# Kernel tuning notes

Measured on AMD Instinct MI355X. Metric: run time of the kernel, lower is better.

The kernel has to match this reference:

```python
import jax, jax.numpy as jnp
import numpy as np

WEIGHT = 1.0  # init kwarg: loss weight
N = 4096
D_FEAT = 128


def _pairwise_dist(x):
    # x: [n, d] -> D: [n, n] Euclidean distances (safe sqrt for grad at 0)
    sq = jnp.sum(x * x, axis=-1)
    d2 = sq[:, None] + sq[None, :] - 2.0 * (x @ x.T)
    d2 = jnp.maximum(d2, 0.0)
    pos = d2 > 1e-12
    return jnp.where(pos, jnp.sqrt(jnp.where(pos, d2, 1.0)), 0.0)


def _prim_mst(D):
    # Vectorized Prim: returns (parents, children) of the n-1 MST edges.
    # filtration value (VR complex truncated at max_dimension=1).
    n = D.shape[0]
    INF = jnp.finfo(D.dtype).max
    visited0 = jnp.zeros(n, dtype=bool).at[0].set(True)
    mind0 = D[0]
    parent0 = jnp.zeros(n, dtype=jnp.int32)

    def step(carry, _):
        visited, mind, parent = carry
        j = jnp.argmin(jnp.where(visited, INF, mind))
        pj = parent[j]
        visited = visited.at[j].set(True)
        better = (D[j] < mind) & (~visited)
        mind = jnp.where(better, D[j], mind)
        parent = jnp.where(better, j, parent)
        return (visited, mind, parent), (pj, j.astype(jnp.int32))

    _, (pjs, js) = jax.lax.scan(step, (visited0, mind0, parent0), None, length=n - 1)
    return pjs, js


def _h1_persistence(x):
    # H1 diagram for VR complex with max_dimension=1: a 1-cycle is born when a
    # non-MST edge appears; with no 2-simplices it never dies, so deaths are
    # capped at the maximal filtration value. Persistence = cap - birth.
    n = x.shape[0]
    D = _pairwise_dist(x)
    pjs, js = _prim_mst(D)
    tree = jnp.zeros((n, n), dtype=bool)
    tree = tree.at[pjs, js].set(True)
    tree = tree | tree.T
    iu = np.triu_indices(n, 1)  # static indices
    births = D[iu]              # [n*(n-1)/2]
    is_tree = tree[iu]
    cap = jnp.max(D)
    # tree edges are H0 (not H1): give them zero persistence (diagonal points)
    return jnp.where(is_tree, 0.0, cap - births)


def _wasserstein_1d(p1, p2):
    # 1-Wasserstein between equal-size persistence multisets via sorted matching
    # (deaths share a common cap per diagram, so matching by sorted persistence).
    return jnp.sum(jnp.abs(jnp.sort(p1) - jnp.sort(p2)))


def setup_inputs() -> dict:
    key = jax.random.key(0)
    k1, k2, k3, k4 = jax.random.split(key, 4)
    return {
        "graph1_features": jax.random.normal(k1, (N, D_FEAT), dtype=jnp.float32),
        "graph1_edges": jax.random.randint(k2, (2, 8 * N), 0, N, dtype=jnp.int64),
        "graph2_features": jax.random.normal(k3, (N, D_FEAT), dtype=jnp.float32),
        "graph2_edges": jax.random.randint(k4, (2, 8 * N), 0, N, dtype=jnp.int64),
    }


def reference(graph1_features, graph1_edges, graph2_features, graph2_edges):
    # edge tensors are unused: the torch forward builds VR complexes from the
    # point clouds only (build_from_points), matching the original module.
    p1 = _h1_persistence(graph1_features)
    p2 = _h1_persistence(graph2_features)
    return WEIGHT * _wasserstein_1d(p1, p2)
```

## Files before the change

### kernel.cpp

```cpp
#include <hip/hip_runtime.h>
#include <stdint.h>

#define NN 4096
#define DF 128
#define NBINS 16384
#define NSLAB 256
#define BORUVKA_ROUNDS 12

typedef __attribute__((ext_vector_type(8))) short short8;
typedef __attribute__((ext_vector_type(4))) float floatx4;
typedef __attribute__((ext_vector_type(4))) unsigned short ushort4_t;
typedef __attribute__((ext_vector_type(4))) int int4_t;

__device__ __forceinline__ unsigned bin_of(float v, float scale) {
  if (v < 0.f) v = 0.f;
  unsigned b = (unsigned)(v * scale);
  return b >= (unsigned)NBINS ? (unsigned)(NBINS - 1) : b;
}

__device__ __forceinline__ void gload16(const unsigned short* g, unsigned short* l) {
  __builtin_amdgcn_global_load_lds(
      (const __attribute__((address_space(1))) void*)g,
      (__attribute__((address_space(3))) void*)l, 16, 0, 0);
}

__global__ void k_rownorm(const float* __restrict__ x1, const float* __restrict__ x2,
                          float* __restrict__ sq) {
  int i = blockIdx.x * blockDim.x + threadIdx.x;
  if (i >= 2 * NN) return;
  const float* x = (i < NN) ? x1 : x2;
  int r = i & (NN - 1);
  const float* row = x + (size_t)r * DF;
  float s = 0.f;
  for (int k = 0; k < DF; ++k) s += row[k] * row[k];
  sq[i] = s;
}

__global__ __launch_bounds__(256) void k_bound(const float* __restrict__ sq,
                                               float* __restrict__ hdrf) {
  int t = threadIdx.x;
  float m = 0.f;
  for (int i = t; i < 2 * NN; i += 256) m = fmaxf(m, sq[i]);
  for (int off = 32; off > 0; off >>= 1) m = fmaxf(m, __shfl_down(m, off, 64));
  __shared__ float wm[4];
  if ((t & 63) == 0) wm[t >> 6] = m;
  __syncthreads();
  if (t == 0) {
    float mm = fmaxf(fmaxf(wm[0], wm[1]), fmaxf(wm[2], wm[3]));
    float dbound = 2.f * sqrtf(mm);
    hdrf[2] = 65535.f / dbound;
    hdrf[3] = dbound / 65535.f;
  }
}

__global__ void k_split(const float* __restrict__ x1, const float* __restrict__ x2,
                        unsigned short* __restrict__ xh, unsigned short* __restrict__ xl) {
  int i = blockIdx.x * blockDim.x + threadIdx.x;
  if (i >= 2 * NN * DF) return;
  const float* x = (i < NN * DF) ? x1 : x2;
  float v = x[i & (NN * DF - 1)];
  unsigned u = __float_as_uint(v);
  unsigned hu = u & 0xffff0000u;
  float hf = __uint_as_float(hu);
  float lf = v - hf;
  unsigned lu = __float_as_uint(lf) & 0xffff0000u;
  xh[i] = (unsigned short)(hu >> 16);
  xl[i] = (unsigned short)(lu >> 16);
}

#define SJ 136
__global__ __launch_bounds__(256) void k_dist(const unsigned short* __restrict__ Xhi,
                                              const unsigned short* __restrict__ Xlo,
                                              const float* __restrict__ sq,
                                              const float* __restrict__ hdrf,
                                              unsigned short* __restrict__ Qbase,
                                              unsigned* __restrict__ caps) {
  int bi = blockIdx.y, bj = blockIdx.x;
  if (bi > bj) return;
  bool offdiag = (bi != bj);
  int g = blockIdx.z;
  const unsigned short* xh = Xhi + (size_t)g * NN * DF;
  const unsigned short* xl = Xlo + (size_t)g * NN * DF;
  const float* sqg = sq + g * NN;
  unsigned short* Q = Qbase + (size_t)g * NN * NN;
  float qs = hdrf[2];
  int t = threadIdx.x;
  int w = t >> 6, lane = t & 63;
  int m = lane & 15, quad = lane >> 4;
  int iw = (w >> 1) * 64, jw = (w & 1) * 64;
  int i0 = bi * 128 + iw;
  int j0 = bj * 128 + jw;

  __shared__ __align__(16) unsigned short SB[128 * SJ];

  int baseRow = (w < 2) ? bi * 128 : bj * 128;
  const unsigned short* src = (w == 0 || w == 2) ? xh : xl;
  unsigned short* ldsPiece = &SB[w * 4096];
  int rsub = lane >> 2;
  int kpart = (lane & 3) ^ ((lane >> 3) & 3);

  int fr = (quad ^ ((m >> 1) & 3)) << 3;

  floatx4 acc[4][4];
#pragma unroll
  for (int ti = 0; ti < 4; ++ti)
#pragma unroll
    for (int tj = 0; tj < 4; ++tj) acc[ti][tj] = (floatx4){0.f, 0.f, 0.f, 0.f};

  for (int s = 0; s < 4; ++s) {
    int kc = s * 32;
    if (s) __syncthreads();
#pragma unroll
    for (int i = 0; i < 8; ++i) {
      const unsigned short* gp =
          src + (size_t)(baseRow + i * 16 + rsub) * DF + kc + kpart * 8;
      gload16(gp, &ldsPiece[i * 512]);
    }
    __syncthreads();
    short8 ah[4], al[4], bh[4], bl[4];
#pragma unroll
    for (int ti = 0; ti < 4; ++ti) {
      int ra = (iw + ti * 16 + m) * 32 + fr;
      int rb = (jw + ti * 16 + m) * 32 + fr;
      ah[ti] = *(const short8*)&SB[ra];
      al[ti] = *(const short8*)&SB[4096 + ra];
      bh[ti] = *(const short8*)&SB[8192 + rb];
      bl[ti] = *(const short8*)&SB[12288 + rb];
    }
#pragma unroll
    for (int ti = 0; ti < 4; ++ti)
#pragma unroll
      for (int tj = 0; tj < 4; ++tj) {
        acc[ti][tj] = __builtin_amdgcn_mfma_f32_16x16x32_bf16(ah[ti], bh[tj], acc[ti][tj], 0, 0, 0);
        acc[ti][tj] = __builtin_amdgcn_mfma_f32_16x16x32_bf16(ah[ti], bl[tj], acc[ti][tj], 0, 0, 0);
        acc[ti][tj] = __builtin_amdgcn_mfma_f32_16x16x32_bf16(al[ti], bh[tj], acc[ti][tj], 0, 0, 0);
      }
  }

  float sqj[4];
#pragma unroll
  for (int tj = 0; tj < 4; ++tj) sqj[tj] = sqg[j0 + tj * 16 + m];
  float mx = 0.f;
  ushort4_t qv[4][4];
#pragma unroll
  for (int ti = 0; ti < 4; ++ti) {
    int ib = i0 + ti * 16 + quad * 4;
    float sqiv[4];
#pragma unroll
    for (int r = 0; r < 4; ++r) sqiv[r] = sqg[ib + r];
#pragma unroll
    for (int tj = 0; tj < 4; ++tj) {
#pragma unroll
      for (int r = 0; r < 4; ++r) {
        float d2 = sqiv[r] + sqj[tj] - 2.f * acc[ti][tj][r];
        d2 = fmaxf(d2, 0.f);
        float d = (d2 > 1e-12f) ? sqrtf(d2) : 0.f;
        mx = fmaxf(mx, d);
        unsigned q = (unsigned)(d * qs + 0.5f);
        if (q > 65535u) q = 65535u;
        qv[ti][tj][r] = (unsigned short)q;
      }
    }
  }

  __syncthreads();
  unsigned short* T = SB;
  int sub = t >> 4, l16 = t & 15;

#pragma unroll
  for (int ti = 0; ti < 4; ++ti) {
    int il = iw + ti * 16 + quad * 4;
#pragma unroll
    for (int tj = 0; tj < 4; ++tj) {
      int jl = jw + tj * 16 + m;
      *(ushort4_t*)&T[jl * SJ + il] = qv[ti][tj];
    }
  }
  __syncthreads();
#pragma unroll
  for (int k = 0; k < 8; ++k) {
    int jl = k * 16 + sub;
    int4_t v = *(const int4_t*)&T[jl * SJ + l16 * 8];
    *(int4_t*)&Q[(size_t)(bj * 128 + jl) * NN + bi * 128 + l16 * 8] = v;
  }

  if (offdiag) {
    __syncthreads();
#pragma unroll
    for (int ti = 0; ti < 4; ++ti) {
      int il = iw + ti * 16 + quad * 4;
#pragma unroll
      for (int tj = 0; tj < 4; ++tj) {
        int jl = jw + tj * 16 + m;
#pragma unroll
        for (int r = 0; r < 4; ++r) T[(il + r) * SJ + jl] = qv[ti][tj][r];
      }
    }
    __syncthreads();
#pragma unroll
    for (int k = 0; k < 8; ++k) {
      int il = k * 16 + sub;
      int4_t v = *(const int4_t*)&T[il * SJ + l16 * 8];
      *(int4_t*)&Q[(size_t)(bi * 128 + il) * NN + bj * 128 + l16 * 8] = v;
    }
  }

  for (int off = 32; off > 0; off >>= 1) mx = fmaxf(mx, __shfl_down(mx, off, 64));
  __shared__ float wmax[4];
  if (lane == 0) wmax[w] = mx;
  __syncthreads();
  if (t == 0) {
    float mm = fmaxf(fmaxf(wmax[0], wmax[1]), fmaxf(wmax[2], wmax[3]));
    atomicMax(&caps[g], __float_as_uint(mm));
  }
}

__global__ void k_binit(int* __restrict__ comp, unsigned long long* __restrict__ compbest,
                        unsigned long long* __restrict__ bestkey,
                        int* __restrict__ mstcnt, int* __restrict__ ncomp) {
  int i = blockIdx.x * blockDim.x + threadIdx.x;
  if (i >= 2 * NN) return;
  comp[i] = i & (NN - 1);
  compbest[i] = ~0ull;
  bestkey[i] = ~0ull;
  if ((i & (NN - 1)) == 0) {
    mstcnt[i >> 12] = 0;
    ncomp[i >> 12] = NN;
  }
}

__global__ __launch_bounds__(256) void k_minedge(const unsigned short* __restrict__ Qbase,
                                                 const int* __restrict__ comp_base,
                                                 unsigned long long* __restrict__ compbest_base,
                                                 unsigned long long* __restrict__ bestkey_base,
                                                 const int* __restrict__ ncomp) {
  int g = blockIdx.y;
  if (ncomp[g] == 1) return;
  int w = threadIdx.x >> 6, lane = threadIdx.x & 63;
  int v = blockIdx.x * 4 + w;
  const int* comp = comp_base + g * NN;
  unsigned long long* cbest = compbest_base + (size_t)g * NN;
  unsigned long long* bkp = bestkey_base + (size_t)g * NN;
  int cv = comp[v];
  unsigned long long bk = bkp[v];
  if (bk != ~0ull) {
    int bj = (int)(bk & 0xfffull);
    if (comp[bj] != cv) {
      if (lane == 0) atomicMin(&cbest[cv], bk);
      return;
    }
  }
  const unsigned short* row = Qbase + ((size_t)g * NN + (size_t)v) * NN;
  unsigned long long best = ~0ull;
#pragma unroll 4
  for (int it = 0; it < NN / 256; ++it) {
    int jb = (it * 64 + lane) * 4;
    ushort4_t rw = *(const ushort4_t*)&row[jb];
    int4_t cj = *(const int4_t*)&comp[jb];
#pragma unroll
    for (int u = 0; u < 4; ++u) {
      if (cj[u] != cv) {
        unsigned long long key = ((unsigned long long)rw[u] << 24) |
                                 ((unsigned long long)v << 12) | (unsigned)(jb + u);
        if (key < best) best = key;
      }
    }
  }
  for (int off = 32; off > 0; off >>= 1) {
    unsigned long long o = __shfl_down(best, off, 64);
    if (o < best) best = o;
  }
  if (lane == 0) {
    bkp[v] = best;
    if (best != ~0ull) atomicMin(&cbest[cv], best);
  }
}

__global__ __launch_bounds__(512) void k_hook(unsigned long long* __restrict__ compbest_base,
                                              int* __restrict__ comp_base,
                                              const float* __restrict__ hdrf,
                                              float* __restrict__ mstw_base,
                                              int* __restrict__ mstcnt,
                                              int* __restrict__ ncomp) {
  int g = blockIdx.x;
  if (ncomp[g] == 1) return;
  unsigned long long* cb = compbest_base + (size_t)g * NN;
  int* comp = comp_base + g * NN;
  float* mstw = mstw_base + g * (NN - 1);
  float qinv = hdrf[3];
  __shared__ int par[NN];
  __shared__ unsigned char live[NN];
  __shared__ int newcnt;
  int t = threadIdx.x;
  if (t == 0) newcnt = 0;
  for (int c = t; c < NN; c += 512) {
    unsigned long long key = cb[c];
    bool a = (key != ~0ull);
    live[c] = a ? 1 : 0;
    int p = c;
    if (a) {
      int j = (int)(key & 0xfffull);
      p = comp[j];
    }
    par[c] = p;
  }
  __syncthreads();
  for (int c = t; c < NN; c += 512) {
    int p = par[c];
    if (p != c && par[p] == c && c < p) par[c] = c;
  }
  __syncthreads();
  for (int c = t; c < NN; c += 512) {
    if (live[c] && par[c] != c) {
      float w = (float)((unsigned)(cb[c] >> 24)) * qinv;
      int slot = atomicAdd(&mstcnt[g], 1);
      mstw[slot] = w;
    }
  }
  __syncthreads();
  for (;;) {
    int np[NN / 512];
    bool ch = false;
    int k = 0;
    for (int c = t; c < NN; c += 512, ++k) {
      int p = par[c];
      int pp = par[p];
      np[k] = pp;
      if (pp != p) ch = true;
    }
    __syncthreads();
    k = 0;
    for (int c = t; c < NN; c += 512, ++k) par[c] = np[k];
    if (!__syncthreads_or(ch)) break;
  }
  int cnt = 0;
  for (int c = t; c < NN; c += 512)
    if (live[c] && par[c] == c) cnt++;
  for (int off = 32; off > 0; off >>= 1) cnt += __shfl_down(cnt, off, 64);
  if ((t & 63) == 0 && cnt) atomicAdd(&newcnt, cnt);
  for (int v = t; v < NN; v += 512) comp[v] = par[comp[v]];
  for (int c = t; c < NN; c += 512) cb[c] = ~0ull;
  __syncthreads();
  if (t == 0) ncomp[g] = newcnt;
}

__global__ __launch_bounds__(256) void k_hist(const unsigned short* __restrict__ Qbase,
                                              const unsigned* __restrict__ caps,
                                              const float* __restrict__ hdrf,
                                              unsigned* __restrict__ Hs) {
  __shared__ unsigned h[NBINS];
  int t = threadIdx.x;
  for (int i = t; i < NBINS; i += 256) h[i] = 0;
  int b = blockIdx.x;
  int g = b >> 8, s = b & (NSLAB - 1);
  const unsigned short* Q = Qbase + (size_t)g * NN * NN;
  float cap = __uint_as_float(caps[g]);
  float capmax = fmaxf(__uint_as_float(caps[0]), __uint_as_float(caps[1]));
  float scale = (float)NBINS / capmax;
  float qinv = hdrf[3];
  __syncthreads();
  for (int p = s; p < NN / 2; p += NSLAB) {
    int r1 = p, r2 = NN - 1 - p;
    const unsigned short* row1 = Q + (size_t)r1 * NN;
    const unsigned short* row2 = Q + (size_t)r2 * NN;
    for (int j = r1 + 1 + t; j < NN; j += 256)
      atomicAdd(&h[bin_of(cap - (float)row1[j] * qinv, scale)], 1u);
    for (int j = r2 + 1 + t; j < NN; j += 256)
      atomicAdd(&h[bin_of(cap - (float)row2[j] * qinv, scale)], 1u);
  }
  __syncthreads();
  unsigned* slab = Hs + (size_t)b * NBINS;
  for (int i = t; i < NBINS; i += 256) slab[i] = h[i];
}

__global__ void k_treefix(const float* __restrict__ twbase, const unsigned* __restrict__ caps,
                          unsigned* __restrict__ Hs) {
  int g = blockIdx.y;
  unsigned* hist = Hs + (size_t)(g * NSLAB) * NBINS;
  float cap = __uint_as_float(caps[g]);
  float capmax = fmaxf(__uint_as_float(caps[0]), __uint_as_float(caps[1]));
  float scale = (float)NBINS / capmax;
  int idx = blockIdx.x * blockDim.x + threadIdx.x;
  if (idx < NN - 1) {
    float w = twbase[g * (NN - 1) + idx];
    atomicSub(&hist[bin_of(cap - w, scale)], 1u);
    atomicAdd(&hist[0], 1u);
  }
}

__global__ __launch_bounds__(256) void k_merge(const unsigned* __restrict__ Hs,
                                               unsigned* __restrict__ Hm) {
  int id = blockIdx.x * 256 + threadIdx.x;
  int g = id >> 14;
  int i = id & (NBINS - 1);
  const unsigned* base = Hs + (size_t)(g * NSLAB) * NBINS + i;
  unsigned sum = 0;
  for (int s = 0; s < NSLAB; ++s) sum += base[(size_t)s * NBINS];
  Hm[id] = sum;
}

__global__ __launch_bounds__(256) void k_w1(const unsigned* __restrict__ Hm,
                                            const unsigned* __restrict__ caps,
                                            float* __restrict__ out) {
  int t = threadIdx.x;
  const int PB = NBINS / 256;
  int base = t * PB;
  long long tsum = 0;
  for (int i = 0; i < PB; ++i)
    tsum += (long long)(int)(Hm[base + i] - Hm[NBINS + base + i]);
  int lane = t & 63, wid = t >> 6;
  long long incl = tsum;
  for (int off = 1; off < 64; off <<= 1) {
    long long o = __shfl_up(incl, off, 64);
    if (lane >= off) incl += o;
  }
  __shared__ long long wtot[4];
  if (lane == 63) wtot[wid] = incl;
  __syncthreads();
  long long run = incl - tsum;
  for (int w = 0; w < wid; ++w) run += wtot[w];
  unsigned long long local = 0;
  for (int i = 0; i < PB; ++i) {
    run += (long long)(int)(Hm[base + i] - Hm[NBINS + base + i]);
    local += (unsigned long long)(run < 0 ? -run : run);
  }
  for (int off = 32; off > 0; off >>= 1) local += __shfl_down(local, off, 64);
  __shared__ unsigned long long wl[4];
  if (lane == 0) wl[wid] = local;
  __syncthreads();
  if (t == 0) {
    float capmax = fmaxf(__uint_as_float(caps[0]), __uint_as_float(caps[1]));
    double dt = (double)capmax / (double)NBINS;
    out[0] = (float)((double)(wl[0] + wl[1] + wl[2] + wl[3]) * dt);
  }
}

__global__ void k_fail(float* out) { out[0] = -1234567.0f; }

extern "C" void kernel_launch(void* const* d_in, const int* in_sizes, int n_in,
                              void* d_out, int out_size, void* d_ws, size_t ws_size,
                              hipStream_t stream) {
  const float* x1 = (const float*)d_in[0];
  const float* x2 = (const float*)d_in[2];
  float* out = (float*)d_out;
  char* ws = (char*)d_ws;

  const size_t offQ = 0;
  const size_t offS = 2ull * NN * NN * 2ull;
  const size_t offHm = offS + 2ull * NSLAB * NBINS * 4ull;
  const size_t offHdr = offHm + 2ull * NBINS * 4ull;
  const size_t offSq = offHdr + 64;
  const size_t offTw = offSq + 2ull * NN * 4ull;
  const size_t offCb = (offTw + 2ull * (NN - 1) * 4ull + 7ull) & ~7ull;
  const size_t offBk = offCb + 2ull * NN * 8ull;
  const size_t offCp = offBk + 2ull * NN * 8ull;
  const size_t offMeta = offCp + 2ull * NN * 4ull;
  const size_t needed = offMeta + 64;
  if (ws_size < needed) {
    hipLaunchKernelGGL(k_fail, dim3(1), dim3(1), 0, stream, out);
    return;
  }

  unsigned short* Qbase = (unsigned short*)(ws + offQ);
  unsigned* Hs = (unsigned*)(ws + offS);
  unsigned short* Xhi = (unsigned short*)(ws + offS);
  unsigned short* Xlo = (unsigned short*)(ws + offS + 2ull * NN * DF * 2ull);
  unsigned* Hm = (unsigned*)(ws + offHm);
  unsigned* caps = (unsigned*)(ws + offHdr);
  float* hdrf = (float*)(ws + offHdr);
  float* sq = (float*)(ws + offSq);
  float* tw = (float*)(ws + offTw);
  unsigned long long* compbest = (unsigned long long*)(ws + offCb);
  unsigned long long* bestkey = (unsigned long long*)(ws + offBk);
  int* comp = (int*)(ws + offCp);
  int* mstcnt = (int*)(ws + offMeta);
  int* ncomp = (int*)(ws + offMeta + 8);

  hipMemsetAsync(ws + offHdr, 0, 64, stream);

  hipLaunchKernelGGL(k_rownorm, dim3((2 * NN + 255) / 256), dim3(256), 0, stream, x1, x2, sq);
  hipLaunchKernelGGL(k_bound, dim3(1), dim3(256), 0, stream, sq, hdrf);
  hipLaunchKernelGGL(k_split, dim3((2 * NN * DF + 255) / 256), dim3(256), 0, stream,
                     x1, x2, Xhi, Xlo);
  hipLaunchKernelGGL(k_dist, dim3(NN / 128, NN / 128, 2), dim3(256), 0, stream,
                     Xhi, Xlo, sq, hdrf, Qbase, caps);
  hipLaunchKernelGGL(k_binit, dim3((2 * NN + 255) / 256), dim3(256), 0, stream,
                     comp, compbest, bestkey, mstcnt, ncomp);
  for (int r = 0; r < BORUVKA_ROUNDS; ++r) {
    hipLaunchKernelGGL(k_minedge, dim3(NN / 4, 2), dim3(256), 0, stream,
                       Qbase, comp, compbest, bestkey, ncomp);
    hipLaunchKernelGGL(k_hook, dim3(2), dim3(512), 0, stream,
                       compbest, comp, hdrf, tw, mstcnt, ncomp);
  }
  hipLaunchKernelGGL(k_hist, dim3(2 * NSLAB), dim3(256), 0, stream, Qbase, caps, hdrf, Hs);
  hipLaunchKernelGGL(k_treefix, dim3(16, 2), dim3(256), 0, stream, tw, caps, Hs);
  hipLaunchKernelGGL(k_merge, dim3(2 * NBINS / 256), dim3(256), 0, stream, Hs, Hm);
  hipLaunchKernelGGL(k_w1, dim3(1), dim3(256), 0, stream, Hm, caps, out);
}
```

Measured before the change: 380.2 us.

## Fuse Boruvka min-edge and hook into one kernel via last-block pattern

Merges the per-round min-edge search and component hooking kernels into a single launch, where the last block to finish (tracked by an atomic counter) performs the hook/pointer-jumping step. This halves the Boruvka kernel launches and the inter-kernel gaps across the 12 rounds. The histogram kernel also switches to 8-wide vectorized row loads with an aligned head. In exchange, every block now reserves the large shared arrays used only by the hook step, which may lower occupancy, and the last block runs the serial hook work while the rest of the grid sits idle.

```diff
diff --git a/kernel.cpp b/kernel.cpp
--- a/kernel.cpp
+++ b/kernel.cpp
@@ -10,6 +10,7 @@
 typedef __attribute__((ext_vector_type(8))) short short8;
 typedef __attribute__((ext_vector_type(4))) float floatx4;
 typedef __attribute__((ext_vector_type(4))) unsigned short ushort4_t;
+typedef __attribute__((ext_vector_type(8))) unsigned short ushort8_t;
 typedef __attribute__((ext_vector_type(4))) int int4_t;
 
 __device__ __forceinline__ unsigned bin_of(float v, float scale) {
@@ -98,7 +99,6 @@
   unsigned short* ldsPiece = &SB[w * 4096];
   int rsub = lane >> 2;
   int kpart = (lane & 3) ^ ((lane >> 3) & 3);
-
   int fr = (quad ^ ((m >> 1) & 3)) << 3;
 
   floatx4 acc[4][4];
@@ -217,92 +217,104 @@
 
 __global__ void k_binit(int* __restrict__ comp, unsigned long long* __restrict__ compbest,
                         unsigned long long* __restrict__ bestkey,
-                        int* __restrict__ mstcnt, int* __restrict__ ncomp) {
+                        int* __restrict__ mstcnt, int* __restrict__ ncomp,
+                        int* __restrict__ done) {
   int i = blockIdx.x * blockDim.x + threadIdx.x;
   if (i >= 2 * NN) return;
   comp[i] = i & (NN - 1);
   compbest[i] = ~0ull;
   bestkey[i] = ~0ull;
   if ((i & (NN - 1)) == 0) {
-    mstcnt[i >> 12] = 0;
-    ncomp[i >> 12] = NN;
-  }
-}
-
-__global__ __launch_bounds__(256) void k_minedge(const unsigned short* __restrict__ Qbase,
-                                                 const int* __restrict__ comp_base,
-                                                 unsigned long long* __restrict__ compbest_base,
-                                                 unsigned long long* __restrict__ bestkey_base,
-                                                 const int* __restrict__ ncomp) {
+    int g = i >> 12;
+    mstcnt[g] = 0;
+    ncomp[g] = NN;
+    done[g] = 0;
+  }
+}
+
+__global__ __launch_bounds__(512) void k_round(
+    const unsigned short* __restrict__ Qbase,
+    int* __restrict__ comp_base,
+    unsigned long long* __restrict__ compbest_base,
+    unsigned long long* __restrict__ bestkey_base,
+    const float* __restrict__ hdrf,
+    float* __restrict__ mstw_base,
+    int* __restrict__ mstcnt,
+    int* __restrict__ ncomp,
+    int* __restrict__ done) {
   int g = blockIdx.y;
   if (ncomp[g] == 1) return;
-  int w = threadIdx.x >> 6, lane = threadIdx.x & 63;
-  int v = blockIdx.x * 4 + w;
-  const int* comp = comp_base + g * NN;
+  int t = threadIdx.x;
+  int w = t >> 6, lane = t & 63;
+  int v = blockIdx.x * 8 + w;
+  int* comp = comp_base + g * NN;
   unsigned long long* cbest = compbest_base + (size_t)g * NN;
   unsigned long long* bkp = bestkey_base + (size_t)g * NN;
-  int cv = comp[v];
-  unsigned long long bk = bkp[v];
-  if (bk != ~0ull) {
-    int bj = (int)(bk & 0xfffull);
-    if (comp[bj] != cv) {
-      if (lane == 0) atomicMin(&cbest[cv], bk);
-      return;
-    }
-  }
-  const unsigned short* row = Qbase + ((size_t)g * NN + (size_t)v) * NN;
-  unsigned long long best = ~0ull;
+
+  {
+    int cv = comp[v];
+    unsigned long long bk = bkp[v];
+    bool need = true;
+    if (bk != ~0ull) {
+      int bj = (int)(bk & 0xfffull);
+      if (comp[bj] != cv) {
+        if (lane == 0) atomicMin(&cbest[cv], bk);
+        need = false;
+      }
+    }
+    if (need) {
+      const unsigned short* row = Qbase + ((size_t)g * NN + (size_t)v) * NN;
+      unsigned long long best = ~0ull;
 #pragma unroll 4
-  for (int it = 0; it < NN / 256; ++it) {
-    int jb = (it * 64 + lane) * 4;
-    ushort4_t rw = *(const ushort4_t*)&row[jb];
-    int4_t cj = *(const int4_t*)&comp[jb];
-#pragma unroll
-    for (int u = 0; u < 4; ++u) {
-      if (cj[u] != cv) {
-        unsigned long long key = ((unsigned long long)rw[u] << 24) |
-                                 ((unsigned long long)v << 12) | (unsigned)(jb + u);
-        if (key < best) best = key;
-      }
-    }
-  }
-  for (int off = 32; off > 0; off >>= 1) {
-    unsigned long long o = __shfl_down(best, off, 64);
-    if (o < best) best = o;
-  }
-  if (lane == 0) {
-    bkp[v] = best;
-    if (best != ~0ull) atomicMin(&cbest[cv], best);
-  }
-}
-
-__global__ __launch_bounds__(512) void k_hook(unsigned long long* __restrict__ compbest_base,
-                                              int* __restrict__ comp_base,
-                                              const float* __restrict__ hdrf,
-                                              float* __restrict__ mstw_base,
-                                              int* __restrict__ mstcnt,
-                                              int* __restrict__ ncomp) {
-  int g = blockIdx.x;
-  if (ncomp[g] == 1) return;
-  unsigned long long* cb = compbest_base + (size_t)g * NN;
-  int* comp = comp_base + g * NN;
+      for (int it = 0; it < NN / 256; ++it) {
+        int jb = (it * 64 + lane) * 4;
+        ushort4_t rw = *(const ushort4_t*)&row[jb];
+        int4_t cj = *(const int4_t*)&comp[jb];
+#pragma unroll
+        for (int u = 0; u < 4; ++u) {
+          if (cj[u] != cv) {
+            unsigned long long key = ((unsigned long long)rw[u] << 24) |
+                                     ((unsigned long long)v << 12) | (unsigned)(jb + u);
+            if (key < best) best = key;
+          }
+        }
+      }
+      for (int off = 32; off > 0; off >>= 1) {
+        unsigned long long o = __shfl_down(best, off, 64);
+        if (o < best) best = o;
+      }
+      if (lane == 0) {
+        bkp[v] = best;
+        if (best != ~0ull) atomicMin(&cbest[cv], best);
+      }
+    }
+  }
+
+  __threadfence();
+  __syncthreads();
+  __shared__ int amlast;
+  if (t == 0) amlast = (atomicAdd(&done[g], 1) == (int)gridDim.x - 1) ? 1 : 0;
+  __syncthreads();
+  if (!amlast) return;
+
+  float qinv = hdrf[3];
+  unsigned long long* cb = cbest;
   float* mstw = mstw_base + g * (NN - 1);
-  float qinv = hdrf[3];
   __shared__ int par[NN];
   __shared__ unsigned char live[NN];
   __shared__ int newcnt;
-  int t = threadIdx.x;
   if (t == 0) newcnt = 0;
   for (int c = t; c < NN; c += 512) {
-    unsigned long long key = cb[c];
+    unsigned long long key =
+        __hip_atomic_load(&cb[c], __ATOMIC_RELAXED, __HIP_MEMORY_SCOPE_AGENT);
     bool a = (key != ~0ull);
     live[c] = a ? 1 : 0;
     int p = c;
+    if (a) p = comp[(int)(key & 0xfffull)];
+    par[c] = p;
     if (a) {
-      int j = (int)(key & 0xfffull);
-      p = comp[j];
-    }
-    par[c] = p;
+      float wgt = (float)((unsigned)(key >> 24)) * qinv;
+    }
   }
   __syncthreads();
   for (int c = t; c < NN; c += 512) {
@@ -312,9 +324,11 @@
   __syncthreads();
   for (int c = t; c < NN; c += 512) {
     if (live[c] && par[c] != c) {
-      float w = (float)((unsigned)(cb[c] >> 24)) * qinv;
+      unsigned long long key =
+          __hip_atomic_load(&cb[c], __ATOMIC_RELAXED, __HIP_MEMORY_SCOPE_AGENT);
+      float wgt = (float)((unsigned)(key >> 24)) * qinv;
       int slot = atomicAdd(&mstcnt[g], 1);
-      mstw[slot] = w;
+      mstw[slot] = wgt;
     }
   }
   __syncthreads();
@@ -338,10 +352,13 @@
     if (live[c] && par[c] == c) cnt++;
   for (int off = 32; off > 0; off >>= 1) cnt += __shfl_down(cnt, off, 64);
   if ((t & 63) == 0 && cnt) atomicAdd(&newcnt, cnt);
-  for (int v = t; v < NN; v += 512) comp[v] = par[comp[v]];
+  for (int u = t; u < NN; u += 512) comp[u] = par[comp[u]];
   for (int c = t; c < NN; c += 512) cb[c] = ~0ull;
   __syncthreads();
-  if (t == 0) ncomp[g] = newcnt;
+  if (t == 0) {
+    ncomp[g] = newcnt;
+    done[g] = 0;
+  }
 }
 
 __global__ __launch_bounds__(256) void k_hist(const unsigned short* __restrict__ Qbase,
@@ -360,13 +377,22 @@
   float qinv = hdrf[3];
   __syncthreads();
   for (int p = s; p < NN / 2; p += NSLAB) {
-    int r1 = p, r2 = NN - 1 - p;
-    const unsigned short* row1 = Q + (size_t)r1 * NN;
-    const unsigned short* row2 = Q + (size_t)r2 * NN;
-    for (int j = r1 + 1 + t; j < NN; j += 256)
-      atomicAdd(&h[bin_of(cap - (float)row1[j] * qinv, scale)], 1u);
-    for (int j = r2 + 1 + t; j < NN; j += 256)
-      atomicAdd(&h[bin_of(cap - (float)row2[j] * qinv, scale)], 1u);
+#pragma unroll
+    for (int half = 0; half < 2; ++half) {
+      int rrow = half ? (NN - 1 - p) : p;
+      const unsigned short* row = Q + (size_t)rrow * NN;
+      int j0 = rrow + 1;
+      int ja = (j0 + 7) & ~7;
+      if (t < ja - j0)
+        atomicAdd(&h[bin_of(cap - (float)row[j0 + t] * qinv, scale)], 1u);
+      int nch = (NN - ja) >> 3;
+      for (int c = t; c < nch; c += 256) {
+        ushort8_t v8 = *(const ushort8_t*)&row[ja + c * 8];
+#pragma unroll
+        for (int u = 0; u < 8; ++u)
+          atomicAdd(&h[bin_of(cap - (float)v8[u] * qinv, scale)], 1u);
+      }
+    }
   }
   __syncthreads();
   unsigned* slab = Hs + (size_t)b * NBINS;
@@ -475,6 +501,7 @@
   int* comp = (int*)(ws + offCp);
   int* mstcnt = (int*)(ws + offMeta);
   int* ncomp = (int*)(ws + offMeta + 8);
+  int* done = (int*)(ws + offMeta + 16);
 
   hipMemsetAsync(ws + offHdr, 0, 64, stream);
 
@@ -485,12 +512,10 @@
   hipLaunchKernelGGL(k_dist, dim3(NN / 128, NN / 128, 2), dim3(256), 0, stream,
                      Xhi, Xlo, sq, hdrf, Qbase, caps);
   hipLaunchKernelGGL(k_binit, dim3((2 * NN + 255) / 256), dim3(256), 0, stream,
-                     comp, compbest, bestkey, mstcnt, ncomp);
+                     comp, compbest, bestkey, mstcnt, ncomp, done);
   for (int r = 0; r < BORUVKA_ROUNDS; ++r) {
-    hipLaunchKernelGGL(k_minedge, dim3(NN / 4, 2), dim3(256), 0, stream,
-                       Qbase, comp, compbest, bestkey, ncomp);
-    hipLaunchKernelGGL(k_hook, dim3(2), dim3(512), 0, stream,
-                       compbest, comp, hdrf, tw, mstcnt, ncomp);
+    hipLaunchKernelGGL(k_round, dim3(NN / 8, 2), dim3(512), 0, stream,
+                       Qbase, comp, compbest, bestkey, hdrf, tw, mstcnt, ncomp, done);
   }
   hipLaunchKernelGGL(k_hist, dim3(2 * NSLAB), dim3(256), 0, stream, Qbase, caps, hdrf, Hs);
   hipLaunchKernelGGL(k_treefix, dim3(16, 2), dim3(256), 0, stream, tw, caps, Hs);
```

Measured after the change: 824.9 us. +116.9%, slower.

## Seed per-vertex nearest neighbor in distance kernel and vectorize histogram row loads

Applied to the files above, without the earlier changes.

The distance GEMM kernel now computes, for each row and column of its tile, the minimum packed (quantized distance, row, col) key and atomically mins it into bestkey. This pre-seeds the first Boruvka round's nearest-neighbor search, so k_minedge can skip a full scan of Q in round one. k_binit is moved before k_dist to initialize bestkey. The histogram kernel also reads Q rows as 16-byte vectors after an aligned prologue. The cost is extra shuffles and 64-bit atomics in the GEMM epilogue.

```diff
diff --git a/kernel.cpp b/kernel.cpp
--- a/kernel.cpp
+++ b/kernel.cpp
@@ -10,6 +10,7 @@
 typedef __attribute__((ext_vector_type(8))) short short8;
 typedef __attribute__((ext_vector_type(4))) float floatx4;
 typedef __attribute__((ext_vector_type(4))) unsigned short ushort4_t;
+typedef __attribute__((ext_vector_type(8))) unsigned short ushort8_t;
 typedef __attribute__((ext_vector_type(4))) int int4_t;
 
 __device__ __forceinline__ unsigned bin_of(float v, float scale) {
@@ -68,12 +69,27 @@
   xl[i] = (unsigned short)(lu >> 16);
 }
 
+__global__ void k_binit(int* __restrict__ comp, unsigned long long* __restrict__ compbest,
+                        unsigned long long* __restrict__ bestkey,
+                        int* __restrict__ mstcnt, int* __restrict__ ncomp) {
+  int i = blockIdx.x * blockDim.x + threadIdx.x;
+  if (i >= 2 * NN) return;
+  comp[i] = i & (NN - 1);
+  compbest[i] = ~0ull;
+  bestkey[i] = ~0ull;
+  if ((i & (NN - 1)) == 0) {
+    mstcnt[i >> 12] = 0;
+    ncomp[i >> 12] = NN;
+  }
+}
+
 #define SJ 136
 __global__ __launch_bounds__(256) void k_dist(const unsigned short* __restrict__ Xhi,
                                               const unsigned short* __restrict__ Xlo,
                                               const float* __restrict__ sq,
                                               const float* __restrict__ hdrf,
                                               unsigned short* __restrict__ Qbase,
+                                              unsigned long long* __restrict__ bestkey_base,
                                               unsigned* __restrict__ caps) {
   int bi = blockIdx.y, bj = blockIdx.x;
   if (bi > bj) return;
@@ -98,7 +114,6 @@
   unsigned short* ldsPiece = &SB[w * 4096];
   int rsub = lane >> 2;
   int kpart = (lane & 3) ^ ((lane >> 3) & 3);
-
   int fr = (quad ^ ((m >> 1) & 3)) << 3;
 
   floatx4 acc[4][4];
@@ -205,6 +220,52 @@
     }
   }
 
+  {
+    unsigned long long* bkp = bestkey_base + (size_t)g * NN;
+#pragma unroll
+    for (int ti = 0; ti < 4; ++ti) {
+#pragma unroll
+      for (int r = 0; r < 4; ++r) {
+        int row = i0 + ti * 16 + quad * 4 + r;
+        unsigned long long kmin = ~0ull;
+#pragma unroll
+        for (int tj = 0; tj < 4; ++tj) {
+          int jj = j0 + tj * 16 + m;
+          unsigned long long key = ((unsigned long long)qv[ti][tj][r] << 24) |
+                                   ((unsigned long long)row << 12) | (unsigned)jj;
+          if (jj != row && key < kmin) kmin = key;
+        }
+#pragma unroll
+        for (int s2 = 1; s2 < 16; s2 <<= 1) {
+          unsigned long long o = __shfl_xor(kmin, s2, 16);
+          if (o < kmin) kmin = o;
+        }
+        if (m == 0 && kmin != ~0ull) atomicMin(&bkp[row], kmin);
+      }
+    }
+#pragma unroll
+    for (int tj = 0; tj < 4; ++tj) {
+      int row = j0 + tj * 16 + m;
+      unsigned long long kmin = ~0ull;
+#pragma unroll
+      for (int ti = 0; ti < 4; ++ti) {
+#pragma unroll
+        for (int r = 0; r < 4; ++r) {
+          int cc = i0 + ti * 16 + quad * 4 + r;
+          unsigned long long key = ((unsigned long long)qv[ti][tj][r] << 24) |
+                                   ((unsigned long long)row << 12) | (unsigned)cc;
+          if (cc != row && key < kmin) kmin = key;
+        }
+      }
+#pragma unroll
+      for (int s2 = 16; s2 < 64; s2 <<= 1) {
+        unsigned long long o = __shfl_xor(kmin, s2, 64);
+        if (o < kmin) kmin = o;
+      }
+      if (quad == 0 && kmin != ~0ull) atomicMin(&bkp[row], kmin);
+    }
+  }
+
   for (int off = 32; off > 0; off >>= 1) mx = fmaxf(mx, __shfl_down(mx, off, 64));
   __shared__ float wmax[4];
   if (lane == 0) wmax[w] = mx;
@@ -212,20 +273,6 @@
   if (t == 0) {
     float mm = fmaxf(fmaxf(wmax[0], wmax[1]), fmaxf(wmax[2], wmax[3]));
     atomicMax(&caps[g], __float_as_uint(mm));
-  }
-}
-
-__global__ void k_binit(int* __restrict__ comp, unsigned long long* __restrict__ compbest,
-                        unsigned long long* __restrict__ bestkey,
-                        int* __restrict__ mstcnt, int* __restrict__ ncomp) {
-  int i = blockIdx.x * blockDim.x + threadIdx.x;
-  if (i >= 2 * NN) return;
-  comp[i] = i & (NN - 1);
-  compbest[i] = ~0ull;
-  bestkey[i] = ~0ull;
-  if ((i & (NN - 1)) == 0) {
-    mstcnt[i >> 12] = 0;
-    ncomp[i >> 12] = NN;
   }
 }
 
@@ -360,13 +407,22 @@
   float qinv = hdrf[3];
   __syncthreads();
   for (int p = s; p < NN / 2; p += NSLAB) {
-    int r1 = p, r2 = NN - 1 - p;
-    const unsigned short* row1 = Q + (size_t)r1 * NN;
-    const unsigned short* row2 = Q + (size_t)r2 * NN;
-    for (int j = r1 + 1 + t; j < NN; j += 256)
-      atomicAdd(&h[bin_of(cap - (float)row1[j] * qinv, scale)], 1u);
-    for (int j = r2 + 1 + t; j < NN; j += 256)
-      atomicAdd(&h[bin_of(cap - (float)row2[j] * qinv, scale)], 1u);
+#pragma unroll
+    for (int half = 0; half < 2; ++half) {
+      int rrow = half ? (NN - 1 - p) : p;
+      const unsigned short* row = Q + (size_t)rrow * NN;
+      int j0 = rrow + 1;
+      int ja = (j0 + 7) & ~7;
+      if (t < ja - j0)
+        atomicAdd(&h[bin_of(cap - (float)row[j0 + t] * qinv, scale)], 1u);
+      int nch = (NN - ja) >> 3;
+      for (int c = t; c < nch; c += 256) {
+        ushort8_t v8 = *(const ushort8_t*)&row[ja + c * 8];
+#pragma unroll
+        for (int u = 0; u < 8; ++u)
+          atomicAdd(&h[bin_of(cap - (float)v8[u] * qinv, scale)], 1u);
+      }
+    }
   }
   __syncthreads();
   unsigned* slab = Hs + (size_t)b * NBINS;
@@ -482,10 +538,10 @@
   hipLaunchKernelGGL(k_bound, dim3(1), dim3(256), 0, stream, sq, hdrf);
   hipLaunchKernelGGL(k_split, dim3((2 * NN * DF + 255) / 256), dim3(256), 0, stream,
                      x1, x2, Xhi, Xlo);
-  hipLaunchKernelGGL(k_dist, dim3(NN / 128, NN / 128, 2), dim3(256), 0, stream,
-                     Xhi, Xlo, sq, hdrf, Qbase, caps);
   hipLaunchKernelGGL(k_binit, dim3((2 * NN + 255) / 256), dim3(256), 0, stream,
                      comp, compbest, bestkey, mstcnt, ncomp);
+  hipLaunchKernelGGL(k_dist, dim3(NN / 128, NN / 128, 2), dim3(256), 0, stream,
+                     Xhi, Xlo, sq, hdrf, Qbase, bestkey, caps);
   for (int r = 0; r < BORUVKA_ROUNDS; ++r) {
     hipLaunchKernelGGL(k_minedge, dim3(NN / 4, 2), dim3(256), 0, stream,
                        Qbase, comp, compbest, bestkey, ncomp);
```

Result: slower. 412.8 us (+8.6%).
